# Performance work log

Hardware: AMD Instinct MI355X
Metric: run time of the kernel (lower is better)

Reference implementation:

```python
import jax, jax.numpy as jnp
import numpy as np

N_SRC1, N_DST1, N_DST2 = 500000, 100000, 20000
IN_F, H_F, N_CLS = 128, 128, 16
E1, E2 = 2000000, 1000000


def setup_inputs() -> dict:
    key = jax.random.key(0)
    ks = jax.random.split(key, 12)
    inp = {
        "x": jax.random.normal(ks[0], (N_SRC1, IN_F), dtype=jnp.float32),
        "src1": jax.random.randint(ks[1], (E1,), 0, N_SRC1, dtype=jnp.int64) if False else jax.random.randint(ks[1], (E1,), 0, N_SRC1),
        "dst1": jax.random.randint(ks[2], (E1,), 0, N_DST1),
        "w1": jax.random.uniform(ks[3], (E1,), dtype=jnp.float32),
        "src2": jax.random.randint(ks[4], (E2,), 0, N_DST1),
        "dst2": jax.random.randint(ks[5], (E2,), 0, N_DST2),
        "w2": jax.random.uniform(ks[6], (E2,), dtype=jnp.float32),
        # SAGEConv params: fc_self (no bias), fc_neigh (+ bias), per DGL
        "W_self1": jax.random.normal(ks[7], (IN_F, H_F), dtype=jnp.float32) / np.sqrt(IN_F),
        "W_neigh1": jax.random.normal(ks[8], (IN_F, H_F), dtype=jnp.float32) / np.sqrt(IN_F),
        "b1": jnp.zeros((H_F,), dtype=jnp.float32),
        "W_self2": jax.random.normal(ks[9], (H_F, N_CLS), dtype=jnp.float32) / np.sqrt(H_F),
        "W_neigh2": jax.random.normal(ks[10], (H_F, N_CLS), dtype=jnp.float32) / np.sqrt(H_F),
        "b2": jnp.zeros((N_CLS,), dtype=jnp.float32),
    }
    return inp


def _sage_mean(h_src, h_dst, src, dst, w, W_self, W_neigh, b, n_dst):
    # message: edge_weight * src feature; aggregate: mean over in-edges of dst
    m = h_src[src] * w[:, None]                             # [E, F]
    s = jax.ops.segment_sum(m, dst, num_segments=n_dst)     # [n_dst, F]
    deg = jax.ops.segment_sum(jnp.ones_like(w), dst, num_segments=n_dst)
    neigh = s / jnp.maximum(deg, 1.0)[:, None]
    return h_dst @ W_self + neigh @ W_neigh + b


def reference(x, src1, dst1, w1, src2, dst2, w2,
              W_self1, W_neigh1, b1, W_self2, W_neigh2, b2):
    h_dst = x[:N_DST1]
    h = _sage_mean(x, h_dst, src1, dst1, w1, W_self1, W_neigh1, b1, N_DST1)
    h = jax.nn.relu(h)
    h_dst2 = h[:N_DST2]
    out = _sage_mean(h, h_dst2, src2, dst2, w2, W_self2, W_neigh2, b2, N_DST2)
    return jax.nn.log_softmax(out, axis=1)
```

## Files before the change

### kernel.cpp

```cpp
#include <hip/hip_runtime.h>

#define NSRC1 500000
#define NDST1 100000
#define NDST2 20000
#define NE1   2000000
#define NE2   1000000
#define F     128
#define NCLS  16
#define C1    56
#define C2    128
#define CONV_BLKS 4096

#define TILE_A 4096
#define NT1 ((NE1 + TILE_A - 1) / TILE_A)
#define NT2 ((NE2 + TILE_A - 1) / TILE_A)
#define BINS1 196
#define BINS2 157
#define CAP1 11264
#define CAP2 7168

typedef float vf4 __attribute__((ext_vector_type(4)));
typedef short short8 __attribute__((ext_vector_type(8)));
typedef float f32x4 __attribute__((ext_vector_type(4)));
typedef unsigned short vus8 __attribute__((ext_vector_type(8)));

#define OFF_BINCUR 0
#define OFF_CNT1   4096
#define OFF_CNT2   404096
#define OFF_WSW    484352
#define OFF_W2SW   549888
#define OFF_SLOT1  554240
#define OFF_G      554240
#define OFF_HSM    6954240
#define OFF_SLOT2  22954240
#define OFF_BIN1   33194240
#define OFF_BIN2   50856192
#define OFF_XB     59859200
#define OFF_NSB    187859200

__device__ __forceinline__ unsigned short f2bf(float f) {
    unsigned u = __float_as_uint(f);
    u = (u + 0x7FFFu + ((u >> 16) & 1u)) >> 16;
    return (unsigned short)u;
}
__device__ __forceinline__ float bfu(unsigned short h) {
    return __uint_as_float(((unsigned)h) << 16);
}

__global__ __launch_bounds__(256) void binA_kernel(
    const int* __restrict__ dst1, const int* __restrict__ src1,
    const float* __restrict__ w1,
    const int* __restrict__ dst2, const int* __restrict__ src2,
    const float* __restrict__ w2,
    int* __restrict__ binCur, int2* __restrict__ bin1, int2* __restrict__ bin2)
{
    __shared__ int hist[BINS1];
    __shared__ int basearr[BINS1];
    int tid = threadIdx.x;
    bool isL2 = blockIdx.x >= NT1;
    int tile = isL2 ? blockIdx.x - NT1 : blockIdx.x;
    const int nb    = isL2 ? BINS2 : BINS1;
    const int shift = isL2 ? 7 : 9;
    const int sb    = isL2 ? 17 : 19;
    const int nE    = isL2 ? NE2 : NE1;
    const int cap   = isL2 ? CAP2 : CAP1;
    const int* dst   = isL2 ? dst2 : dst1;
    const int* src   = isL2 ? src2 : src1;
    const float* w   = isL2 ? w2 : w1;
    int2* bout       = isL2 ? bin2 : bin1;
    int* cur         = binCur + (isL2 ? BINS1 : 0);

    for (int i = tid; i < nb; i += 256) hist[i] = 0;
    __syncthreads();

    int base = tile * TILE_A;
    int key[16]; float wv[16]; int bn[16];
#pragma unroll
    for (int k = 0; k < 16; ++k) {
        int t = base + k * 256 + tid;
        if (t < nE) {
            int d = dst[t];
            int b = d >> shift;
            bn[k] = b;
            key[k] = src[t] | ((d & ((1 << shift) - 1)) << sb);
            wv[k] = w[t];
            atomicAdd(&hist[b], 1);
        } else bn[k] = -1;
    }
    __syncthreads();
    for (int i = tid; i < nb; i += 256) {
        int c = hist[i];
        basearr[i] = c ? atomicAdd(&cur[i], c) : 0;
        hist[i] = 0;
    }
    __syncthreads();
#pragma unroll
    for (int k = 0; k < 16; ++k) {
        if (bn[k] >= 0) {
            int r = atomicAdd(&hist[bn[k]], 1);
            int p = basearr[bn[k]] + r;
            if (p < cap)
                bout[(size_t)bn[k] * cap + p] = make_int2(key[k], __float_as_int(wv[k]));
        }
    }
}

__global__ __launch_bounds__(256) void binB_kernel(
    const int* __restrict__ binCur,
    const int2* __restrict__ bin1, const int2* __restrict__ bin2,
    unsigned* __restrict__ slot1, unsigned* __restrict__ slot2,
    int* __restrict__ cnt1, int* __restrict__ cnt2)
{
    __shared__ int pos[512];
    int tid = threadIdx.x;
    if (blockIdx.x < BINS1) {
        int b = blockIdx.x;
        for (int i = tid; i < 512; i += 256) pos[i] = 0;
        __syncthreads();
        int n = min(binCur[b], CAP1);
        const int2* ptr = bin1 + (size_t)b * CAP1;
        for (int i = tid; i < n; i += 256) {
            int2 rec = ptr[i];
            int dlow = ((unsigned)rec.x) >> 19;
            int s = rec.x & 0x7FFFF;
            float wf = __int_as_float(rec.y);
            int p = atomicAdd(&pos[dlow], 1);
            if (p < C1) {
                unsigned wq = min((unsigned)(wf * 8192.0f), 8191u);
                slot1[(size_t)((b << 9) | dlow) * C1 + p] = ((unsigned)s << 13) | wq;
            }
        }
        __syncthreads();
        for (int i = tid; i < 512; i += 256) {
            int d = (b << 9) + i;
            if (d < NDST1) cnt1[d] = pos[i];
        }
    } else {
        int b = blockIdx.x - BINS1;
        if (tid < 128) pos[tid] = 0;
        __syncthreads();
        int n = min(binCur[BINS1 + b], CAP2);
        const int2* ptr = bin2 + (size_t)b * CAP2;
        for (int i = tid; i < n; i += 256) {
            int2 rec = ptr[i];
            int dlow = ((unsigned)rec.x) >> 17;
            int s = rec.x & 0x1FFFF;
            float wf = __int_as_float(rec.y);
            int p = atomicAdd(&pos[dlow], 1);
            if (p < C2) {
                unsigned wq = min((unsigned)(wf * 32768.0f), 32767u);
                slot2[(((size_t)((b << 7) | dlow)) << 7) + p] = ((unsigned)s << 15) | wq;
            }
        }
        __syncthreads();
        if (tid < 128) {
            int d = (b << 7) + tid;
            if (d < NDST2) cnt2[d] = pos[tid];
        }
    }
}

__global__ __launch_bounds__(256) void conv_kernel(
    const vf4* __restrict__ x4, ushort4* __restrict__ xb)
{
    const long n = (long)NSRC1 * F / 4;
    const long stride = (long)CONV_BLKS * 256;
    long i = (long)blockIdx.x * 256 + threadIdx.x;
    while (i + 3 * stride < n) {
        vf4 v0 = __builtin_nontemporal_load(&x4[i]);
        vf4 v1 = __builtin_nontemporal_load(&x4[i + stride]);
        vf4 v2 = __builtin_nontemporal_load(&x4[i + 2 * stride]);
        vf4 v3 = __builtin_nontemporal_load(&x4[i + 3 * stride]);
        ushort4 o0, o1, o2, o3;
        o0.x = f2bf(v0.x); o0.y = f2bf(v0.y); o0.z = f2bf(v0.z); o0.w = f2bf(v0.w);
        o1.x = f2bf(v1.x); o1.y = f2bf(v1.y); o1.z = f2bf(v1.z); o1.w = f2bf(v1.w);
        o2.x = f2bf(v2.x); o2.y = f2bf(v2.y); o2.z = f2bf(v2.z); o2.w = f2bf(v2.w);
        o3.x = f2bf(v3.x); o3.y = f2bf(v3.y); o3.z = f2bf(v3.z); o3.w = f2bf(v3.w);
        xb[i] = o0;
        xb[i + stride] = o1;
        xb[i + 2 * stride] = o2;
        xb[i + 3 * stride] = o3;
        i += 4 * stride;
    }
    for (; i < n; i += stride) {
        vf4 v = __builtin_nontemporal_load(&x4[i]);
        ushort4 o;
        o.x = f2bf(v.x); o.y = f2bf(v.y); o.z = f2bf(v.z); o.w = f2bf(v.w);
        xb[i] = o;
    }
}

__global__ __launch_bounds__(256) void wsw_kernel(
    const float* __restrict__ Ws1, const float* __restrict__ Wn1,
    const float* __restrict__ Wn2,
    short8* __restrict__ wsw, short8* __restrict__ w2sw)
{
    int wb = blockIdx.x, tid = threadIdx.x;
    if (wb < 16) {
        int e = wb * 256 + tid;
        int l = e & 63, st = e >> 6;
        int t = st & 7, s = st >> 3;
        short8 o;
#pragma unroll
        for (int i = 0; i < 8; ++i) {
            int k = s * 32 + (l >> 4) * 8 + i;
            int n = t * 16 + (l & 15);
            float v = (k < F) ? Ws1[k * F + n] : Wn1[(k - F) * F + n];
            o[i] = (short)f2bf(v);
        }
        wsw[e] = o;
    } else {
        int l = tid & 63, s2 = tid >> 6;
        short8 o;
#pragma unroll
        for (int i = 0; i < 8; ++i) {
            int k = s2 * 32 + (l >> 4) * 8 + i;
            o[i] = (short)f2bf(Wn2[k * NCLS + (l & 15)]);
        }
        w2sw[s2 * 64 + l] = o;
    }
}

__global__ __launch_bounds__(256, 6) void gather1_kernel(
    const vus8* __restrict__ xb8, const unsigned* __restrict__ slot1,
    const int* __restrict__ cnt1, short8* __restrict__ nsb8)
{
    int tid = threadIdx.x;
    int grp = tid >> 4, j = tid & 15;
    int row = blockIdx.x * 16 + grp;
    int deg = cnt1[row];
    int n = min(deg, C1);
    const unsigned* bucket = slot1 + (size_t)row * C1;
    float a[8] = {0.f, 0.f, 0.f, 0.f, 0.f, 0.f, 0.f, 0.f};
    int nb = (n + 7) >> 3;
    unsigned e[8];
    if (nb > 0) {
#pragma unroll
        for (int q = 0; q < 8; ++q) e[q] = bucket[min(q, n - 1)];
    }
    for (int bi = 0; bi < nb; ++bi) {
        int base = bi * 8;
        float wq[8];
        vus8 v[8];
#pragma unroll
        for (int q = 0; q < 8; ++q) {
            wq[q] = (base + q < n) ? ((float)(e[q] & 8191u) + 0.5f) * (1.0f / 8192.0f) : 0.f;
            v[q] = xb8[(size_t)(e[q] >> 13) * 16 + j];
        }
        if (bi + 1 < nb) {
            int nbase = base + 8;
#pragma unroll
            for (int q = 0; q < 8; ++q) e[q] = bucket[min(nbase + q, n - 1)];
        }
#pragma unroll
        for (int q = 0; q < 8; ++q) {
#pragma unroll
            for (int k = 0; k < 8; ++k)
                a[k] += bfu(v[q][k]) * wq[q];
        }
    }
    float invd = 1.0f / fmaxf((float)deg, 1.0f);
    short8 o;
#pragma unroll
    for (int k = 0; k < 8; ++k) o[k] = (short)f2bf(a[k] * invd);
    nsb8[(size_t)row * 16 + j] = o;
}

__global__ __launch_bounds__(256) void dense1_kernel(
    const short8* __restrict__ xb8, const short8* __restrict__ nsb8,
    const short8* __restrict__ wsw, const short8* __restrict__ w2sw,
    const float* __restrict__ b1, float* __restrict__ hsmall,
    float* __restrict__ g)
{
    __shared__ short lds_a[64 * 256];
    short8* la8 = (short8*)lds_a;

    int tid = threadIdx.x;
    int wv = tid >> 6, l = tid & 63;
    int r0 = blockIdx.x * 64;

    for (int it = tid; it < 2048; it += 256) {
        int r = it >> 5, c = it & 31;
        int grow = min(r0 + r, NDST1 - 1);
        short8 v = (c < 16) ? xb8[(size_t)grow * 16 + c]
                            : nsb8[(size_t)grow * 16 + (c - 16)];
        la8[r * 32 + (c ^ (r & 7))] = v;
    }
    __syncthreads();

    int lq = l >> 4;
    int lrow = wv * 16 + (l & 15);
    int lbase = lrow * 32;
    int lkey = lrow & 7;

    f32x4 acc[8];
#pragma unroll
    for (int t = 0; t < 8; ++t) acc[t] = (f32x4){0.f, 0.f, 0.f, 0.f};

#pragma unroll
    for (int s = 0; s < 8; ++s) {
        short8 af = la8[lbase + ((s * 4 + lq) ^ lkey)];
#pragma unroll
        for (int t = 0; t < 8; ++t) {
            short8 bf_ = wsw[(s * 8 + t) * 64 + l];
            acc[t] = __builtin_amdgcn_mfma_f32_16x16x32_bf16(af, bf_, acc[t], 0, 0, 0);
        }
    }
    __syncthreads();

    int orow_base = r0 + wv * 16 + lq * 4;
#pragma unroll
    for (int t = 0; t < 8; ++t) {
        float bv = b1[t * 16 + (l & 15)];
        int col = t * 16 + (l & 15);
        int chunk = col >> 3;
#pragma unroll
        for (int r = 0; r < 4; ++r) {
            float hv = fmaxf(acc[t][r] + bv, 0.f);
            int lr = wv * 16 + lq * 4 + r;
            lds_a[lr * 256 + ((chunk ^ (lr & 7)) << 3) + (col & 7)] = (short)f2bf(hv);
            int orow = orow_base + r;
            if (orow < NDST2) hsmall[(size_t)orow * F + col] = hv;
        }
    }
    __syncthreads();

    f32x4 acc2 = (f32x4){0.f, 0.f, 0.f, 0.f};
#pragma unroll
    for (int s2 = 0; s2 < 4; ++s2) {
        short8 af = la8[lbase + ((s2 * 4 + lq) ^ lkey)];
        short8 bf_ = w2sw[s2 * 64 + l];
        acc2 = __builtin_amdgcn_mfma_f32_16x16x32_bf16(af, bf_, acc2, 0, 0, 0);
    }
#pragma unroll
    for (int r = 0; r < 4; ++r) {
        int orow = orow_base + r;
        if (orow < NDST1) g[(size_t)orow * NCLS + (l & 15)] = acc2[r];
    }
}

__global__ __launch_bounds__(256) void dense2_kernel(
    const float* __restrict__ hsmall, const float* __restrict__ g,
    const unsigned* __restrict__ slot2, const int* __restrict__ cnt2,
    const float* __restrict__ Ws2, const float* __restrict__ b2,
    float* __restrict__ out)
{
    __shared__ float ws[F * NCLS];
    __shared__ float hsh[16][F + 1];
    int tid = threadIdx.x;
    for (int i = tid; i < F * NCLS / 4; i += 256)
        ((float4*)ws)[i] = ((const float4*)Ws2)[i];
    int r0 = blockIdx.x * 16;
    for (int it = tid; it < 16 * 32; it += 256) {
        int r = it >> 5, c = it & 31;
        *(float4*)&hsh[r][c * 4] = ((const float4*)hsmall)[(size_t)(r0 + r) * 32 + c];
    }
    __syncthreads();

    int grp = tid >> 4, j = tid & 15;
    int row = r0 + grp;
    int deg = cnt2[row];
    int n = min(deg, C2);
    const unsigned* bucket = slot2 + ((size_t)row << 7);
    float acc = 0.f;
    int nb = (n + 7) >> 3;
    unsigned e[8];
    if (nb > 0) {
#pragma unroll
        for (int q = 0; q < 8; ++q) e[q] = bucket[min(q, n - 1)];
    }
    for (int bi = 0; bi < nb; ++bi) {
        int base = bi * 8;
        float wq[8], gv[8];
#pragma unroll
        for (int q = 0; q < 8; ++q) {
            wq[q] = (base + q < n) ? ((float)(e[q] & 32767u) + 0.5f) * (1.0f / 32768.0f) : 0.f;
            gv[q] = g[(size_t)(e[q] >> 15) * NCLS + j];
        }
        if (bi + 1 < nb) {
            int nbase = base + 8;
#pragma unroll
            for (int q = 0; q < 8; ++q) e[q] = bucket[min(nbase + q, n - 1)];
        }
#pragma unroll
        for (int q = 0; q < 8; ++q) acc += gv[q] * wq[q];
    }
    float invd = 1.0f / fmaxf((float)deg, 1.0f);
    float v = b2[j] + acc * invd;
#pragma unroll 8
    for (int k = 0; k < F; ++k)
        v += hsh[grp][k] * ws[k * NCLS + j];

    float m = v;
    for (int o = 8; o >= 1; o >>= 1) m = fmaxf(m, __shfl_xor(m, o, 16));
    float s = expf(v - m);
    for (int o = 8; o >= 1; o >>= 1) s += __shfl_xor(s, o, 16);
    out[(size_t)row * NCLS + j] = v - m - logf(s);
}

extern "C" void kernel_launch(void* const* d_in, const int* in_sizes, int n_in,
                              void* d_out, int out_size, void* d_ws, size_t ws_size,
                              hipStream_t stream)
{
    const float* x    = (const float*)d_in[0];
    const int*   src1 = (const int*)d_in[1];
    const int*   dst1 = (const int*)d_in[2];
    const float* w1   = (const float*)d_in[3];
    const int*   src2 = (const int*)d_in[4];
    const int*   dst2 = (const int*)d_in[5];
    const float* w2   = (const float*)d_in[6];
    const float* Ws1  = (const float*)d_in[7];
    const float* Wn1  = (const float*)d_in[8];
    const float* b1   = (const float*)d_in[9];
    const float* Ws2  = (const float*)d_in[10];
    const float* Wn2  = (const float*)d_in[11];
    const float* b2   = (const float*)d_in[12];
    float* out = (float*)d_out;

    char* wsb = (char*)d_ws;
    int*      binCur = (int*)(wsb + OFF_BINCUR);
    int*      cnt1   = (int*)(wsb + OFF_CNT1);
    int*      cnt2   = (int*)(wsb + OFF_CNT2);
    short8*   wsw    = (short8*)(wsb + OFF_WSW);
    short8*   w2sw   = (short8*)(wsb + OFF_W2SW);
    unsigned* slot1  = (unsigned*)(wsb + OFF_SLOT1);
    unsigned* slot2  = (unsigned*)(wsb + OFF_SLOT2);
    int2*     bin1   = (int2*)(wsb + OFF_BIN1);
    int2*     bin2   = (int2*)(wsb + OFF_BIN2);
    float*    g      = (float*)(wsb + OFF_G);
    float*    hsmall = (float*)(wsb + OFF_HSM);
    ushort4*  xb     = (ushort4*)(wsb + OFF_XB);
    short8*   nsb    = (short8*)(wsb + OFF_NSB);

    (void)hipMemsetAsync(d_ws, 0, 4096, stream);

    binA_kernel<<<NT1 + NT2, 256, 0, stream>>>(
        dst1, src1, w1, dst2, src2, w2, binCur, bin1, bin2);

    conv_kernel<<<CONV_BLKS, 256, 0, stream>>>((const vf4*)x, xb);

    wsw_kernel<<<17, 256, 0, stream>>>(Ws1, Wn1, Wn2, wsw, w2sw);

    binB_kernel<<<BINS1 + BINS2, 256, 0, stream>>>(
        binCur, bin1, bin2, slot1, slot2, cnt1, cnt2);

    gather1_kernel<<<NDST1 / 16, 256, 0, stream>>>(
        (const vus8*)xb, slot1, cnt1, nsb);

    dense1_kernel<<<(NDST1 + 63) / 64, 256, 0, stream>>>(
        (const short8*)xb, nsb, wsw, w2sw, b1, hsmall, g);

    dense2_kernel<<<NDST2 / 16, 256, 0, stream>>>(
        hsmall, g, slot2, cnt2, Ws2, b2, out);
}
```

Before: 276.6 us.

## Fuse neighbor gather into dense1 and merge prep kernels

Gathers the layer-1 neighbor mean directly into shared memory inside the dense GEMM kernel. This drops the intermediate nsb buffer and its global write and read. The binning and fp32-to-bf16 conversion kernels are merged into one launch, and the weight swizzle is combined with zeroing binCur, which replaces the memset. This cuts launches and intermediate traffic, but the fused kernel now has only 1563 blocks doing a latency-bound gather, so occupancy and latency hiding for the gather may be worse than with the separate 6250-block launch.

```diff
diff --git a/kernel.cpp b/kernel.cpp
--- a/kernel.cpp
+++ b/kernel.cpp
@@ -36,7 +36,6 @@
 #define OFF_BIN1   33194240
 #define OFF_BIN2   50856192
 #define OFF_XB     59859200
-#define OFF_NSB    187859200
 
 __device__ __forceinline__ unsigned short f2bf(float f) {
     unsigned u = __float_as_uint(f);
@@ -47,60 +46,123 @@
     return __uint_as_float(((unsigned)h) << 16);
 }
 
-__global__ __launch_bounds__(256) void binA_kernel(
+__global__ __launch_bounds__(256) void prep0_kernel(
+    const float* __restrict__ Ws1, const float* __restrict__ Wn1,
+    const float* __restrict__ Wn2,
+    short8* __restrict__ wsw, short8* __restrict__ w2sw,
+    int* __restrict__ binCur)
+{
+    int wb = blockIdx.x, tid = threadIdx.x;
+    if (wb < 16) {
+        int e = wb * 256 + tid;
+        int l = e & 63, st = e >> 6;
+        int t = st & 7, s = st >> 3;
+        short8 o;
+#pragma unroll
+        for (int i = 0; i < 8; ++i) {
+            int k = s * 32 + (l >> 4) * 8 + i;
+            int n = t * 16 + (l & 15);
+            float v = (k < F) ? Ws1[k * F + n] : Wn1[(k - F) * F + n];
+            o[i] = (short)f2bf(v);
+        }
+        wsw[e] = o;
+    } else if (wb == 16) {
+        int l = tid & 63, s2 = tid >> 6;
+        short8 o;
+#pragma unroll
+        for (int i = 0; i < 8; ++i) {
+            int k = s2 * 32 + (l >> 4) * 8 + i;
+            o[i] = (short)f2bf(Wn2[k * NCLS + (l & 15)]);
+        }
+        w2sw[s2 * 64 + l] = o;
+    } else {
+        for (int i = tid; i < 1024; i += 256) binCur[i] = 0;
+    }
+}
+
+__global__ __launch_bounds__(256) void prepA_kernel(
     const int* __restrict__ dst1, const int* __restrict__ src1,
     const float* __restrict__ w1,
     const int* __restrict__ dst2, const int* __restrict__ src2,
     const float* __restrict__ w2,
-    int* __restrict__ binCur, int2* __restrict__ bin1, int2* __restrict__ bin2)
-{
-    __shared__ int hist[BINS1];
-    __shared__ int basearr[BINS1];
+    int* __restrict__ binCur, int2* __restrict__ bin1, int2* __restrict__ bin2,
+    const vf4* __restrict__ x4, ushort4* __restrict__ xb)
+{
     int tid = threadIdx.x;
-    bool isL2 = blockIdx.x >= NT1;
-    int tile = isL2 ? blockIdx.x - NT1 : blockIdx.x;
-    const int nb    = isL2 ? BINS2 : BINS1;
-    const int shift = isL2 ? 7 : 9;
-    const int sb    = isL2 ? 17 : 19;
-    const int nE    = isL2 ? NE2 : NE1;
-    const int cap   = isL2 ? CAP2 : CAP1;
-    const int* dst   = isL2 ? dst2 : dst1;
-    const int* src   = isL2 ? src2 : src1;
-    const float* w   = isL2 ? w2 : w1;
-    int2* bout       = isL2 ? bin2 : bin1;
-    int* cur         = binCur + (isL2 ? BINS1 : 0);
-
-    for (int i = tid; i < nb; i += 256) hist[i] = 0;
-    __syncthreads();
-
-    int base = tile * TILE_A;
-    int key[16]; float wv[16]; int bn[16];
-#pragma unroll
-    for (int k = 0; k < 16; ++k) {
-        int t = base + k * 256 + tid;
-        if (t < nE) {
-            int d = dst[t];
-            int b = d >> shift;
-            bn[k] = b;
-            key[k] = src[t] | ((d & ((1 << shift) - 1)) << sb);
-            wv[k] = w[t];
-            atomicAdd(&hist[b], 1);
-        } else bn[k] = -1;
-    }
-    __syncthreads();
-    for (int i = tid; i < nb; i += 256) {
-        int c = hist[i];
-        basearr[i] = c ? atomicAdd(&cur[i], c) : 0;
-        hist[i] = 0;
-    }
-    __syncthreads();
-#pragma unroll
-    for (int k = 0; k < 16; ++k) {
-        if (bn[k] >= 0) {
-            int r = atomicAdd(&hist[bn[k]], 1);
-            int p = basearr[bn[k]] + r;
-            if (p < cap)
-                bout[(size_t)bn[k] * cap + p] = make_int2(key[k], __float_as_int(wv[k]));
+    if (blockIdx.x < NT1 + NT2) {
+        __shared__ int hist[BINS1];
+        __shared__ int basearr[BINS1];
+        bool isL2 = blockIdx.x >= NT1;
+        int tile = isL2 ? blockIdx.x - NT1 : blockIdx.x;
+        const int nb    = isL2 ? BINS2 : BINS1;
+        const int shift = isL2 ? 7 : 9;
+        const int sb    = isL2 ? 17 : 19;
+        const int nE    = isL2 ? NE2 : NE1;
+        const int cap   = isL2 ? CAP2 : CAP1;
+        const int* dst   = isL2 ? dst2 : dst1;
+        const int* src   = isL2 ? src2 : src1;
+        const float* w   = isL2 ? w2 : w1;
+        int2* bout       = isL2 ? bin2 : bin1;
+        int* cur         = binCur + (isL2 ? BINS1 : 0);
+
+        for (int i = tid; i < nb; i += 256) hist[i] = 0;
+        __syncthreads();
+
+        int base = tile * TILE_A;
+        int key[16]; float wv[16]; int bn[16];
+#pragma unroll
+        for (int k = 0; k < 16; ++k) {
+            int t = base + k * 256 + tid;
+            if (t < nE) {
+                int d = dst[t];
+                int b = d >> shift;
+                bn[k] = b;
+                key[k] = src[t] | ((d & ((1 << shift) - 1)) << sb);
+                wv[k] = w[t];
+                atomicAdd(&hist[b], 1);
+            } else bn[k] = -1;
+        }
+        __syncthreads();
+        for (int i = tid; i < nb; i += 256) {
+            int c = hist[i];
+            basearr[i] = c ? atomicAdd(&cur[i], c) : 0;
+            hist[i] = 0;
+        }
+        __syncthreads();
+#pragma unroll
+        for (int k = 0; k < 16; ++k) {
+            if (bn[k] >= 0) {
+                int r = atomicAdd(&hist[bn[k]], 1);
+                int p = basearr[bn[k]] + r;
+                if (p < cap)
+                    bout[(size_t)bn[k] * cap + p] = make_int2(key[k], __float_as_int(wv[k]));
+            }
+        }
+    } else {
+        const long n = (long)NSRC1 * F / 4;
+        const long stride = (long)CONV_BLKS * 256;
+        long i = (long)(blockIdx.x - NT1 - NT2) * 256 + tid;
+        while (i + 3 * stride < n) {
+            vf4 v0 = __builtin_nontemporal_load(&x4[i]);
+            vf4 v1 = __builtin_nontemporal_load(&x4[i + stride]);
+            vf4 v2 = __builtin_nontemporal_load(&x4[i + 2 * stride]);
+            vf4 v3 = __builtin_nontemporal_load(&x4[i + 3 * stride]);
+            ushort4 o0, o1, o2, o3;
+            o0.x = f2bf(v0.x); o0.y = f2bf(v0.y); o0.z = f2bf(v0.z); o0.w = f2bf(v0.w);
+            o1.x = f2bf(v1.x); o1.y = f2bf(v1.y); o1.z = f2bf(v1.z); o1.w = f2bf(v1.w);
+            o2.x = f2bf(v2.x); o2.y = f2bf(v2.y); o2.z = f2bf(v2.z); o2.w = f2bf(v2.w);
+            o3.x = f2bf(v3.x); o3.y = f2bf(v3.y); o3.z = f2bf(v3.z); o3.w = f2bf(v3.w);
+            xb[i] = o0;
+            xb[i + stride] = o1;
+            xb[i + 2 * stride] = o2;
+            xb[i + 3 * stride] = o3;
+            i += 4 * stride;
+        }
+        for (; i < n; i += stride) {
+            vf4 v = __builtin_nontemporal_load(&x4[i]);
+            ushort4 o;
+            o.x = f2bf(v.x); o.y = f2bf(v.y); o.z = f2bf(v.z); o.w = f2bf(v.w);
+            xb[i] = o;
         }
     }
 }
@@ -160,114 +222,9 @@
     }
 }
 
-__global__ __launch_bounds__(256) void conv_kernel(
-    const vf4* __restrict__ x4, ushort4* __restrict__ xb)
-{
-    const long n = (long)NSRC1 * F / 4;
-    const long stride = (long)CONV_BLKS * 256;
-    long i = (long)blockIdx.x * 256 + threadIdx.x;
-    while (i + 3 * stride < n) {
-        vf4 v0 = __builtin_nontemporal_load(&x4[i]);
-        vf4 v1 = __builtin_nontemporal_load(&x4[i + stride]);
-        vf4 v2 = __builtin_nontemporal_load(&x4[i + 2 * stride]);
-        vf4 v3 = __builtin_nontemporal_load(&x4[i + 3 * stride]);
-        ushort4 o0, o1, o2, o3;
-        o0.x = f2bf(v0.x); o0.y = f2bf(v0.y); o0.z = f2bf(v0.z); o0.w = f2bf(v0.w);
-        o1.x = f2bf(v1.x); o1.y = f2bf(v1.y); o1.z = f2bf(v1.z); o1.w = f2bf(v1.w);
-        o2.x = f2bf(v2.x); o2.y = f2bf(v2.y); o2.z = f2bf(v2.z); o2.w = f2bf(v2.w);
-        o3.x = f2bf(v3.x); o3.y = f2bf(v3.y); o3.z = f2bf(v3.z); o3.w = f2bf(v3.w);
-        xb[i] = o0;
-        xb[i + stride] = o1;
-        xb[i + 2 * stride] = o2;
-        xb[i + 3 * stride] = o3;
-        i += 4 * stride;
-    }
-    for (; i < n; i += stride) {
-        vf4 v = __builtin_nontemporal_load(&x4[i]);
-        ushort4 o;
-        o.x = f2bf(v.x); o.y = f2bf(v.y); o.z = f2bf(v.z); o.w = f2bf(v.w);
-        xb[i] = o;
-    }
-}
-
-__global__ __launch_bounds__(256) void wsw_kernel(
-    const float* __restrict__ Ws1, const float* __restrict__ Wn1,
-    const float* __restrict__ Wn2,
-    short8* __restrict__ wsw, short8* __restrict__ w2sw)
-{
-    int wb = blockIdx.x, tid = threadIdx.x;
-    if (wb < 16) {
-        int e = wb * 256 + tid;
-        int l = e & 63, st = e >> 6;
-        int t = st & 7, s = st >> 3;
-        short8 o;
-#pragma unroll
-        for (int i = 0; i < 8; ++i) {
-            int k = s * 32 + (l >> 4) * 8 + i;
-            int n = t * 16 + (l & 15);
-            float v = (k < F) ? Ws1[k * F + n] : Wn1[(k - F) * F + n];
-            o[i] = (short)f2bf(v);
-        }
-        wsw[e] = o;
-    } else {
-        int l = tid & 63, s2 = tid >> 6;
-        short8 o;
-#pragma unroll
-        for (int i = 0; i < 8; ++i) {
-            int k = s2 * 32 + (l >> 4) * 8 + i;
-            o[i] = (short)f2bf(Wn2[k * NCLS + (l & 15)]);
-        }
-        w2sw[s2 * 64 + l] = o;
-    }
-}
-
-__global__ __launch_bounds__(256, 6) void gather1_kernel(
-    const vus8* __restrict__ xb8, const unsigned* __restrict__ slot1,
-    const int* __restrict__ cnt1, short8* __restrict__ nsb8)
-{
-    int tid = threadIdx.x;
-    int grp = tid >> 4, j = tid & 15;
-    int row = blockIdx.x * 16 + grp;
-    int deg = cnt1[row];
-    int n = min(deg, C1);
-    const unsigned* bucket = slot1 + (size_t)row * C1;
-    float a[8] = {0.f, 0.f, 0.f, 0.f, 0.f, 0.f, 0.f, 0.f};
-    int nb = (n + 7) >> 3;
-    unsigned e[8];
-    if (nb > 0) {
-#pragma unroll
-        for (int q = 0; q < 8; ++q) e[q] = bucket[min(q, n - 1)];
-    }
-    for (int bi = 0; bi < nb; ++bi) {
-        int base = bi * 8;
-        float wq[8];
-        vus8 v[8];
-#pragma unroll
-        for (int q = 0; q < 8; ++q) {
-            wq[q] = (base + q < n) ? ((float)(e[q] & 8191u) + 0.5f) * (1.0f / 8192.0f) : 0.f;
-            v[q] = xb8[(size_t)(e[q] >> 13) * 16 + j];
-        }
-        if (bi + 1 < nb) {
-            int nbase = base + 8;
-#pragma unroll
-            for (int q = 0; q < 8; ++q) e[q] = bucket[min(nbase + q, n - 1)];
-        }
-#pragma unroll
-        for (int q = 0; q < 8; ++q) {
-#pragma unroll
-            for (int k = 0; k < 8; ++k)
-                a[k] += bfu(v[q][k]) * wq[q];
-        }
-    }
-    float invd = 1.0f / fmaxf((float)deg, 1.0f);
-    short8 o;
-#pragma unroll
-    for (int k = 0; k < 8; ++k) o[k] = (short)f2bf(a[k] * invd);
-    nsb8[(size_t)row * 16 + j] = o;
-}
-
-__global__ __launch_bounds__(256) void dense1_kernel(
-    const short8* __restrict__ xb8, const short8* __restrict__ nsb8,
+__global__ __launch_bounds__(256) void dense1f_kernel(
+    const short8* __restrict__ xb8, const vus8* __restrict__ xbv,
+    const unsigned* __restrict__ slot1, const int* __restrict__ cnt1,
     const short8* __restrict__ wsw, const short8* __restrict__ w2sw,
     const float* __restrict__ b1, float* __restrict__ hsmall,
     float* __restrict__ g)
@@ -279,12 +236,54 @@
     int wv = tid >> 6, l = tid & 63;
     int r0 = blockIdx.x * 64;
 
-    for (int it = tid; it < 2048; it += 256) {
-        int r = it >> 5, c = it & 31;
+    for (int it = tid; it < 1024; it += 256) {
+        int r = it >> 4, c = it & 15;
         int grow = min(r0 + r, NDST1 - 1);
-        short8 v = (c < 16) ? xb8[(size_t)grow * 16 + c]
-                            : nsb8[(size_t)grow * 16 + (c - 16)];
-        la8[r * 32 + (c ^ (r & 7))] = v;
+        la8[r * 32 + (c ^ (r & 7))] = xb8[(size_t)grow * 16 + c];
+    }
+
+    {
+        int grp = tid >> 4, j = tid & 15;
+        for (int rr = 0; rr < 4; ++rr) {
+            int rloc = rr * 16 + grp;
+            int row = min(r0 + rloc, NDST1 - 1);
+            int deg = cnt1[row];
+            int n = min(deg, C1);
+            const unsigned* bucket = slot1 + (size_t)row * C1;
+            float a[8] = {0.f, 0.f, 0.f, 0.f, 0.f, 0.f, 0.f, 0.f};
+            int nb = (n + 7) >> 3;
+            unsigned e[8];
+            if (nb > 0) {
+#pragma unroll
+                for (int q = 0; q < 8; ++q) e[q] = bucket[min(q, n - 1)];
+            }
+            for (int bi = 0; bi < nb; ++bi) {
+                int base = bi * 8;
+                float wq[8];
+                vus8 v[8];
+#pragma unroll
+                for (int q = 0; q < 8; ++q) {
+                    wq[q] = (base + q < n) ? ((float)(e[q] & 8191u) + 0.5f) * (1.0f / 8192.0f) : 0.f;
+                    v[q] = xbv[(size_t)(e[q] >> 13) * 16 + j];
+                }
+                if (bi + 1 < nb) {
+                    int nbase = base + 8;
+#pragma unroll
+                    for (int q = 0; q < 8; ++q) e[q] = bucket[min(nbase + q, n - 1)];
+                }
+#pragma unroll
+                for (int q = 0; q < 8; ++q) {
+#pragma unroll
+                    for (int k = 0; k < 8; ++k)
+                        a[k] += bfu(v[q][k]) * wq[q];
+                }
+            }
+            float invd = 1.0f / fmaxf((float)deg, 1.0f);
+            short8 o;
+#pragma unroll
+            for (int k = 0; k < 8; ++k) o[k] = (short)f2bf(a[k] * invd);
+            la8[rloc * 32 + ((16 + j) ^ (rloc & 7))] = o;
+        }
     }
     __syncthreads();
 
@@ -430,25 +429,17 @@
     float*    g      = (float*)(wsb + OFF_G);
     float*    hsmall = (float*)(wsb + OFF_HSM);
     ushort4*  xb     = (ushort4*)(wsb + OFF_XB);
-    short8*   nsb    = (short8*)(wsb + OFF_NSB);
-
-    (void)hipMemsetAsync(d_ws, 0, 4096, stream);
-
-    binA_kernel<<<NT1 + NT2, 256, 0, stream>>>(
-        dst1, src1, w1, dst2, src2, w2, binCur, bin1, bin2);
-
-    conv_kernel<<<CONV_BLKS, 256, 0, stream>>>((const vf4*)x, xb);
-
-    wsw_kernel<<<17, 256, 0, stream>>>(Ws1, Wn1, Wn2, wsw, w2sw);
+
+    prep0_kernel<<<18, 256, 0, stream>>>(Ws1, Wn1, Wn2, wsw, w2sw, binCur);
+
+    prepA_kernel<<<NT1 + NT2 + CONV_BLKS, 256, 0, stream>>>(
+        dst1, src1, w1, dst2, src2, w2, binCur, bin1, bin2, (const vf4*)x, xb);
 
     binB_kernel<<<BINS1 + BINS2, 256, 0, stream>>>(
         binCur, bin1, bin2, slot1, slot2, cnt1, cnt2);
 
-    gather1_kernel<<<NDST1 / 16, 256, 0, stream>>>(
-        (const vus8*)xb, slot1, cnt1, nsb);
-
-    dense1_kernel<<<(NDST1 + 63) / 64, 256, 0, stream>>>(
-        (const short8*)xb, nsb, wsw, w2sw, b1, hsmall, g);
+    dense1f_kernel<<<(NDST1 + 63) / 64, 256, 0, stream>>>(
+        (const short8*)xb, (const vus8*)xb, slot1, cnt1, wsw, w2sw, b1, hsmall, g);
 
     dense2_kernel<<<NDST2 / 16, 256, 0, stream>>>(
         hsmall, g, slot2, cnt2, Ws2, b2, out);
```

Measured after the change: 249.4 us. 9.8% less time.
